# Optimization experiments

Measured on AMD Instinct MI355X. Metric: run time of the kernel, lower is better.

The kernel has to match this reference:

```python
import jax, jax.numpy as jnp
import numpy as np

B, N, DX, DZ = 4, 2048, 2, 128
PPD = (128, 128)
GRID_RANGE = ((-2.0, 2.0), (-2.0, 2.0))
INIT_LS = 0.1


def _construct_grid():
    axes = [jnp.linspace(lo, hi, p, dtype=jnp.float32) for (lo, hi), p in zip(GRID_RANGE, PPD)]
    mesh = jnp.meshgrid(*axes, indexing="ij")
    return jnp.stack(mesh, axis=-1)  # [128, 128, 2]


def setup_inputs() -> dict:
    key = jax.random.key(0)
    k1, k2 = jax.random.split(key)
    x = jax.random.uniform(k1, (B, N, DX), dtype=jnp.float32, minval=-2.0, maxval=2.0)
    z = jax.random.normal(k2, (B, N, DZ), dtype=jnp.float32)
    grid = _construct_grid()
    # inverse-softplus of init lengthscale, per dim
    ls0 = jnp.full((DX,), INIT_LS, dtype=jnp.float32)
    lengthscale_param = jnp.log(jnp.exp(ls0) - 1.0)
    return {"x": x, "z": z, "grid": grid, "lengthscale_param": lengthscale_param}


def reference(x, z, grid, lengthscale_param):
    b = x.shape[0]
    grid_shape = grid.shape[:-1]  # (128, 128)
    lengthscale = 1e-05 + jax.nn.softplus(lengthscale_param)  # [dx]
    grid_flat = grid.reshape(-1, grid.shape[-1])  # [M, dx], M = 16384
    # per-dim squared distance / l^2, summed over dx  -> [b, M, n]
    diff = grid_flat[None, :, None, :] - x[:, None, :, :]  # [b, M, n, dx]
    pre_exp = jnp.sum((diff * diff) / (lengthscale ** 2), axis=-1)
    weights = jnp.exp(-0.5 * pre_exp)  # [b, M, n]
    z_grid_flat = jnp.einsum("bmn,bnd->bmd", weights, z)  # [b, M, dz]
    z_grid = z_grid_flat.reshape((b,) + grid_shape + (z.shape[-1],))
    x_grid = jnp.broadcast_to(grid[None], (b,) + grid.shape)
    return (x_grid, z_grid)
```

## Files before the change

kernel.cpp:

```cpp
#include <hip/hip_runtime.h>

#define BATCH 4
#define NPTS  2048
#define DZDIM 128
#define GD    128
#define M_TOT (GD*GD)
#define TN    32
#define PZ    40
#define ZP    2112
#define WBIN  15

typedef __attribute__((ext_vector_type(8))) __bf16 bf16x8;
typedef __attribute__((ext_vector_type(4))) float floatx4;

__device__ __forceinline__ unsigned int f2bf_bits(float x){
  unsigned int u = __float_as_uint(x);
  u += 0x7FFFu + ((u >> 16) & 1u);
  return u >> 16;
}
__device__ __forceinline__ int point_bin(float px){
  int bin = __float2int_rn((px + 2.0f) * (127.0f / 4.0f));
  return min(GD - 1, max(0, bin));
}

__global__ __launch_bounds__(256) void prep_kernel(
    const float* __restrict__ x, const float* __restrict__ grid,
    float* __restrict__ out, int* __restrict__ binStart,
    float2* __restrict__ xs, int* __restrict__ perm)
{
  const int tid = threadIdx.x;
  if (blockIdx.x < BATCH){
    __shared__ int h[GD];
    __shared__ int s[GD + 1];
    const int b = blockIdx.x;
    const float2* __restrict__ x2 = (const float2*)x;
    if (tid < GD) h[tid] = 0;
    __syncthreads();
    float2 xv[8]; int bn[8];
#pragma unroll
    for (int u = 0; u < 8; ++u){
      xv[u] = x2[b*NPTS + u*256 + tid];
      bn[u] = point_bin(xv[u].x);
      atomicAdd(&h[bn[u]], 1);
    }
    __syncthreads();
    if (tid == 0){
      int acc = 0;
#pragma unroll
      for (int j = 0; j < GD; ++j){ s[j] = acc; acc += h[j]; }
      s[GD] = acc;
    }
    __syncthreads();
    if (tid <= GD) binStart[b*(GD+1) + tid] = s[tid];
    if (tid < GD) h[tid] = 0;
    __syncthreads();
#pragma unroll
    for (int u = 0; u < 8; ++u){
      int j = s[bn[u]] + atomicAdd(&h[bn[u]], 1);
      xs[(long)b*ZP + j]       = xv[u];
      perm[b*NPTS + j]         = u*256 + tid;
    }
  } else {
    int idx = (blockIdx.x - BATCH) * 256 + tid;
    float g = grid[idx];
#pragma unroll
    for (int bb = 0; bb < BATCH; ++bb) out[bb*(GD*GD*2) + idx] = g;
  }
}

__global__ __launch_bounds__(256) void ztwy_kernel(
    const float* __restrict__ z, const float2* __restrict__ xs,
    const int* __restrict__ perm, const float* __restrict__ lsp,
    unsigned short* __restrict__ zt, float* __restrict__ wy)
{
  const int b   = blockIdx.y;
  const int jj  = threadIdx.x & 31;
  const int oct = threadIdx.x >> 5;
  if (blockIdx.x >= NPTS/32){
    int j = NPTS + (blockIdx.x - NPTS/32)*32 + jj;
#pragma unroll
    for (int yy = 0; yy < 16; ++yy)
      wy[(long)(b*GD + oct*16 + yy)*ZP + j] = 0.f;
    return;
  }
  const int j = blockIdx.x*32 + jj;
  const int n = perm[b*NPTS + j];
  const float4* __restrict__ z4 = (const float4*)z;
  const long rb = (long)(b*NPTS + n) * 32;
#pragma unroll
  for (int r = 0; r < 4; ++r){
    int c = oct*4 + r;
    float4 v = z4[rb + c];
    long o = ((long)(b*DZDIM + 4*c) * ZP) + j;
    zt[o        ] = (unsigned short)f2bf_bits(v.x);
    zt[o +   ZP ] = (unsigned short)f2bf_bits(v.y);
    zt[o + 2*ZP ] = (unsigned short)f2bf_bits(v.z);
    zt[o + 3*ZP ] = (unsigned short)f2bf_bits(v.w);
  }
  const float l1 = 1e-5f + log1pf(expf(lsp[1]));
  const float c1 = -0.5f * 1.4426950408889634f / (l1*l1);
  const float step = 4.0f / 127.0f;
  const float y = xs[(long)b*ZP + j].y;
  float gy = -2.0f + (float)(oct*16) * step;
#pragma unroll
  for (int yy = 0; yy < 16; ++yy){
    float d = gy - y;
    wy[(long)(b*GD + oct*16 + yy)*ZP + j] = __builtin_amdgcn_exp2f(c1*d*d);
    gy += step;
  }
}

__global__ __launch_bounds__(256, 2) void setconv_mfma_kernel(
    const float2* __restrict__ xs, const int* __restrict__ binStart,
    const unsigned short* __restrict__ zt, const float* __restrict__ wy,
    const float* __restrict__ lsp, float* __restrict__ outz)
{
  __shared__ __align__(16) unsigned short Zlds[2][DZDIM * PZ];
  __shared__ __align__(16) float Wx[2][TN];

  const int tid = threadIdx.x, lane = tid & 63, wv = tid >> 6;
  const int bid = blockIdx.x;
  const int g   = bid & 7;
  const int s   = bid >> 3;
  const int b   = s & 3;
  const int il  = s >> 2;
  const int i   = g*16 + il;

  const float l0 = 1e-5f + log1pf(expf(lsp[0]));
  const float c0 = -0.5f * 1.4426950408889634f / (l0*l0);
  const float step = 4.0f / 127.0f;
  const float gx   = -2.0f + (float)i * step;

  const int lo  = binStart[b*(GD+1) + max(0, i - WBIN)];
  const int hi  = binStart[b*(GD+1) + min(GD-1, i + WBIN) + 1];
  const int lo8 = lo & ~7;
  const int len = hi - lo8;
  const int T   = (len + TN - 1) / TN;

  int goff[3];
#pragma unroll
  for (int u = 0; u < 3; ++u){
    int gi = wv + 4*u;
    if (gi < 10){
      int pos = gi*64 + lane;
      int d = pos / 5, c = pos % 5;
      if (c > 3) c = 3;
      goff[u] = (b*DZDIM + d) * ZP + c*8;
    } else goff[u] = 0;
  }

  const int q  = lane >> 4;
  const int ml = lane & 15;
  const float* __restrict__ wyp = wy + (long)(b*GD + wv*16 + ml) * ZP + q*8;

  floatx4 acc[2][8];
#pragma unroll
  for (int hh = 0; hh < 2; ++hh)
#pragma unroll
    for (int tz = 0; tz < 8; ++tz) acc[hh][tz] = (floatx4){0.f, 0.f, 0.f, 0.f};

  auto stageZ = [&](int buf, int t){
    const int k0 = lo8 + t*TN;
#pragma unroll
    for (int u = 0; u < 3; ++u){
      int gi = wv + 4*u;
      if (gi < 10){
        const unsigned short* gp = zt + goff[u] + k0;
        __builtin_amdgcn_global_load_lds(
            (__attribute__((address_space(1))) void*)gp,
            (__attribute__((address_space(3))) void*)&Zlds[buf][gi*512],
            16, 0, 0);
      }
    }
  };
  auto stageWx = [&](int buf, int t){
    if (tid < TN){
      int ka = t*TN + tid;
      float2 xv = xs[(long)b*ZP + lo8 + ka];
      float d = gx - xv.x;
      float w = __builtin_amdgcn_exp2f(c0*d*d);
      Wx[buf][tid] = (ka < len) ? w : 0.f;
    }
  };

  if (T > 0){
    stageZ(0, 0);
    stageWx(0, 0);
    floatx4 wA0 = *(const floatx4*)(wyp + lo8);
    floatx4 wB0 = *(const floatx4*)(wyp + lo8 + 4);
    floatx4 wA1 = *(const floatx4*)(wyp + 64*ZP + lo8);
    floatx4 wB1 = *(const floatx4*)(wyp + 64*ZP + lo8 + 4);
    __syncthreads();
    for (int t = 0; t < T; ++t){
      const int cur = t & 1, nxt = 1 - cur;
      if (t + 1 < T){ stageZ(nxt, t + 1); stageWx(nxt, t + 1); }
      const int tp = (t + 1 < T) ? t + 1 : t;
      floatx4 nA0 = *(const floatx4*)(wyp + lo8 + tp*TN);
      floatx4 nB0 = *(const floatx4*)(wyp + lo8 + tp*TN + 4);
      floatx4 nA1 = *(const floatx4*)(wyp + 64*ZP + lo8 + tp*TN);
      floatx4 nB1 = *(const floatx4*)(wyp + 64*ZP + lo8 + tp*TN + 4);
      floatx4 wx0 = *(const floatx4*)&Wx[cur][q*8];
      floatx4 wx1 = *(const floatx4*)&Wx[cur][q*8 + 4];
      union { unsigned int u[4]; bf16x8 v; } A0, A1;
      {
        float p0 = wA0[0]*wx0[0], p1 = wA0[1]*wx0[1], p2 = wA0[2]*wx0[2], p3 = wA0[3]*wx0[3];
        float p4 = wB0[0]*wx1[0], p5 = wB0[1]*wx1[1], p6 = wB0[2]*wx1[2], p7 = wB0[3]*wx1[3];
        asm("v_cvt_pk_bf16_f32 %0, %1, %2" : "=v"(A0.u[0]) : "v"(p0), "v"(p1));
        asm("v_cvt_pk_bf16_f32 %0, %1, %2" : "=v"(A0.u[1]) : "v"(p2), "v"(p3));
        asm("v_cvt_pk_bf16_f32 %0, %1, %2" : "=v"(A0.u[2]) : "v"(p4), "v"(p5));
        asm("v_cvt_pk_bf16_f32 %0, %1, %2" : "=v"(A0.u[3]) : "v"(p6), "v"(p7));
      }
      {
        float p0 = wA1[0]*wx0[0], p1 = wA1[1]*wx0[1], p2 = wA1[2]*wx0[2], p3 = wA1[3]*wx0[3];
        float p4 = wB1[0]*wx1[0], p5 = wB1[1]*wx1[1], p6 = wB1[2]*wx1[2], p7 = wB1[3]*wx1[3];
        asm("v_cvt_pk_bf16_f32 %0, %1, %2" : "=v"(A1.u[0]) : "v"(p0), "v"(p1));
        asm("v_cvt_pk_bf16_f32 %0, %1, %2" : "=v"(A1.u[1]) : "v"(p2), "v"(p3));
        asm("v_cvt_pk_bf16_f32 %0, %1, %2" : "=v"(A1.u[2]) : "v"(p4), "v"(p5));
        asm("v_cvt_pk_bf16_f32 %0, %1, %2" : "=v"(A1.u[3]) : "v"(p6), "v"(p7));
      }
      bf16x8 af0 = A0.v, af1 = A1.v;
#pragma unroll
      for (int tz = 0; tz < 8; ++tz){
        bf16x8 bf = *(const bf16x8*)&Zlds[cur][(tz*16 + ml)*PZ + q*8];
        acc[0][tz] = __builtin_amdgcn_mfma_f32_16x16x32_bf16(af0, bf, acc[0][tz], 0, 0, 0);
        acc[1][tz] = __builtin_amdgcn_mfma_f32_16x16x32_bf16(af1, bf, acc[1][tz], 0, 0, 0);
      }
      __syncthreads();
      wA0 = nA0; wB0 = nB0; wA1 = nA1; wB1 = nB1;
    }
  }

#pragma unroll
  for (int hh = 0; hh < 2; ++hh){
    const long obase = ((long)(b*M_TOT + i*GD + hh*64 + wv*16 + q*4) << 7) + ml;
#pragma unroll
    for (int tz = 0; tz < 8; ++tz)
#pragma unroll
      for (int r = 0; r < 4; ++r)
        outz[obase + ((long)r << 7) + tz*16] = acc[hh][tz][r];
  }
}

extern "C" void kernel_launch(void* const* d_in, const int* in_sizes, int n_in,
                              void* d_out, int out_size, void* d_ws, size_t ws_size,
                              hipStream_t stream)
{
  const float* x    = (const float*)d_in[0];
  const float* z    = (const float*)d_in[1];
  const float* grid = (const float*)d_in[2];
  const float* lsp  = (const float*)d_in[3];
  float* out = (float*)d_out;

  char* ws = (char*)d_ws;
  int*            binStart = (int*)ws;
  int*            perm     = (int*)(ws + 2064);
  float2*         xs       = (float2*)(ws + 34832);
  unsigned short* zt       = (unsigned short*)(ws + 102416);
  float*          wy       = (float*)(ws + 2265104);

  hipLaunchKernelGGL(prep_kernel, dim3(BATCH + GD), dim3(256), 0, stream,
                     x, grid, out, binStart, xs, perm);
  hipLaunchKernelGGL(ztwy_kernel, dim3(NPTS/32 + 2, BATCH), dim3(256), 0, stream,
                     z, xs, perm, lsp, zt, wy);
  hipLaunchKernelGGL(setconv_mfma_kernel, dim3(GD*BATCH), dim3(256), 0, stream,
                     xs, binStart, zt, wy, lsp, out + BATCH*GD*GD*2);
}
```

Before: 106.6 us.

## Compute Gaussian weights on the fly inside MFMA kernel instead of precomputed wy table

Removes the precomputed y-direction weight table (written by the z-transpose kernel and streamed from global memory each tile). The main MFMA kernel now stages the sorted point coordinates into LDS and evaluates the full 2D Gaussian weight with one exp2 per element directly in registers. This trades global memory traffic of about 4.3 MB of wy writes and reads for extra exp2 and FMA work per MFMA tile. It also removes the zero-padding blocks from the preceding kernel.

```diff
diff --git a/kernel.cpp b/kernel.cpp
--- a/kernel.cpp
+++ b/kernel.cpp
@@ -68,21 +68,13 @@
   }
 }
 
-__global__ __launch_bounds__(256) void ztwy_kernel(
-    const float* __restrict__ z, const float2* __restrict__ xs,
-    const int* __restrict__ perm, const float* __restrict__ lsp,
-    unsigned short* __restrict__ zt, float* __restrict__ wy)
+__global__ __launch_bounds__(256) void ztbuild_kernel(
+    const float* __restrict__ z, const int* __restrict__ perm,
+    unsigned short* __restrict__ zt)
 {
   const int b   = blockIdx.y;
   const int jj  = threadIdx.x & 31;
   const int oct = threadIdx.x >> 5;
-  if (blockIdx.x >= NPTS/32){
-    int j = NPTS + (blockIdx.x - NPTS/32)*32 + jj;
-#pragma unroll
-    for (int yy = 0; yy < 16; ++yy)
-      wy[(long)(b*GD + oct*16 + yy)*ZP + j] = 0.f;
-    return;
-  }
   const int j = blockIdx.x*32 + jj;
   const int n = perm[b*NPTS + j];
   const float4* __restrict__ z4 = (const float4*)z;
@@ -97,26 +89,15 @@
     zt[o + 2*ZP ] = (unsigned short)f2bf_bits(v.z);
     zt[o + 3*ZP ] = (unsigned short)f2bf_bits(v.w);
   }
-  const float l1 = 1e-5f + log1pf(expf(lsp[1]));
-  const float c1 = -0.5f * 1.4426950408889634f / (l1*l1);
-  const float step = 4.0f / 127.0f;
-  const float y = xs[(long)b*ZP + j].y;
-  float gy = -2.0f + (float)(oct*16) * step;
-#pragma unroll
-  for (int yy = 0; yy < 16; ++yy){
-    float d = gy - y;
-    wy[(long)(b*GD + oct*16 + yy)*ZP + j] = __builtin_amdgcn_exp2f(c1*d*d);
-    gy += step;
-  }
 }
 
 __global__ __launch_bounds__(256, 2) void setconv_mfma_kernel(
     const float2* __restrict__ xs, const int* __restrict__ binStart,
-    const unsigned short* __restrict__ zt, const float* __restrict__ wy,
-    const float* __restrict__ lsp, float* __restrict__ outz)
+    const unsigned short* __restrict__ zt, const float* __restrict__ lsp,
+    float* __restrict__ outz)
 {
   __shared__ __align__(16) unsigned short Zlds[2][DZDIM * PZ];
-  __shared__ __align__(16) float Wx[2][TN];
+  __shared__ __align__(16) float2 XS[2][TN];
 
   const int tid = threadIdx.x, lane = tid & 63, wv = tid >> 6;
   const int bid = blockIdx.x;
@@ -127,7 +108,10 @@
   const int i   = g*16 + il;
 
   const float l0 = 1e-5f + log1pf(expf(lsp[0]));
-  const float c0 = -0.5f * 1.4426950408889634f / (l0*l0);
+  const float l1 = 1e-5f + log1pf(expf(lsp[1]));
+  const float LOG2E = 1.4426950408889634f;
+  const float c0 = -0.5f * LOG2E / (l0*l0);
+  const float c1 = -0.5f * LOG2E / (l1*l1);
   const float step = 4.0f / 127.0f;
   const float gx   = -2.0f + (float)i * step;
 
@@ -151,7 +135,8 @@
 
   const int q  = lane >> 4;
   const int ml = lane & 15;
-  const float* __restrict__ wyp = wy + (long)(b*GD + wv*16 + ml) * ZP + q*8;
+  const float gy0 = -2.0f + (float)(wv*16 + ml) * step;
+  const float gy1 = gy0 + 64.0f * step;
 
   floatx4 acc[2][8];
 #pragma unroll
@@ -173,51 +158,40 @@
       }
     }
   };
-  auto stageWx = [&](int buf, int t){
-    if (tid < TN){
-      int ka = t*TN + tid;
-      float2 xv = xs[(long)b*ZP + lo8 + ka];
-      float d = gx - xv.x;
-      float w = __builtin_amdgcn_exp2f(c0*d*d);
-      Wx[buf][tid] = (ka < len) ? w : 0.f;
-    }
+  auto stageXS = [&](int buf, int t){
+    if (tid < TN)
+      XS[buf][tid] = xs[(long)b*ZP + lo8 + t*TN + tid];
   };
 
   if (T > 0){
     stageZ(0, 0);
-    stageWx(0, 0);
-    floatx4 wA0 = *(const floatx4*)(wyp + lo8);
-    floatx4 wB0 = *(const floatx4*)(wyp + lo8 + 4);
-    floatx4 wA1 = *(const floatx4*)(wyp + 64*ZP + lo8);
-    floatx4 wB1 = *(const floatx4*)(wyp + 64*ZP + lo8 + 4);
+    stageXS(0, 0);
     __syncthreads();
     for (int t = 0; t < T; ++t){
       const int cur = t & 1, nxt = 1 - cur;
-      if (t + 1 < T){ stageZ(nxt, t + 1); stageWx(nxt, t + 1); }
-      const int tp = (t + 1 < T) ? t + 1 : t;
-      floatx4 nA0 = *(const floatx4*)(wyp + lo8 + tp*TN);
-      floatx4 nB0 = *(const floatx4*)(wyp + lo8 + tp*TN + 4);
-      floatx4 nA1 = *(const floatx4*)(wyp + 64*ZP + lo8 + tp*TN);
-      floatx4 nB1 = *(const floatx4*)(wyp + 64*ZP + lo8 + tp*TN + 4);
-      floatx4 wx0 = *(const floatx4*)&Wx[cur][q*8];
-      floatx4 wx1 = *(const floatx4*)&Wx[cur][q*8 + 4];
+      if (t + 1 < T){ stageZ(nxt, t + 1); stageXS(nxt, t + 1); }
+      float w0[8], w1[8];
+#pragma unroll
+      for (int r = 0; r < 8; ++r){
+        float2 p = XS[cur][q*8 + r];
+        float dx = gx - p.x;
+        float t0 = c0*dx*dx;
+        float dy0 = gy0 - p.y, dy1 = gy1 - p.y;
+        float a0 = fmaf(c1*dy0, dy0, t0);
+        float a1 = fmaf(c1*dy1, dy1, t0);
+        bool ok = (t*TN + q*8 + r) < len;
+        w0[r] = ok ? __builtin_amdgcn_exp2f(a0) : 0.f;
+        w1[r] = ok ? __builtin_amdgcn_exp2f(a1) : 0.f;
+      }
       union { unsigned int u[4]; bf16x8 v; } A0, A1;
-      {
-        float p0 = wA0[0]*wx0[0], p1 = wA0[1]*wx0[1], p2 = wA0[2]*wx0[2], p3 = wA0[3]*wx0[3];
-        float p4 = wB0[0]*wx1[0], p5 = wB0[1]*wx1[1], p6 = wB0[2]*wx1[2], p7 = wB0[3]*wx1[3];
-        asm("v_cvt_pk_bf16_f32 %0, %1, %2" : "=v"(A0.u[0]) : "v"(p0), "v"(p1));
-        asm("v_cvt_pk_bf16_f32 %0, %1, %2" : "=v"(A0.u[1]) : "v"(p2), "v"(p3));
-        asm("v_cvt_pk_bf16_f32 %0, %1, %2" : "=v"(A0.u[2]) : "v"(p4), "v"(p5));
-        asm("v_cvt_pk_bf16_f32 %0, %1, %2" : "=v"(A0.u[3]) : "v"(p6), "v"(p7));
-      }
-      {
-        float p0 = wA1[0]*wx0[0], p1 = wA1[1]*wx0[1], p2 = wA1[2]*wx0[2], p3 = wA1[3]*wx0[3];
-        float p4 = wB1[0]*wx1[0], p5 = wB1[1]*wx1[1], p6 = wB1[2]*wx1[2], p7 = wB1[3]*wx1[3];
-        asm("v_cvt_pk_bf16_f32 %0, %1, %2" : "=v"(A1.u[0]) : "v"(p0), "v"(p1));
-        asm("v_cvt_pk_bf16_f32 %0, %1, %2" : "=v"(A1.u[1]) : "v"(p2), "v"(p3));
-        asm("v_cvt_pk_bf16_f32 %0, %1, %2" : "=v"(A1.u[2]) : "v"(p4), "v"(p5));
-        asm("v_cvt_pk_bf16_f32 %0, %1, %2" : "=v"(A1.u[3]) : "v"(p6), "v"(p7));
-      }
+      asm("v_cvt_pk_bf16_f32 %0, %1, %2" : "=v"(A0.u[0]) : "v"(w0[0]), "v"(w0[1]));
+      asm("v_cvt_pk_bf16_f32 %0, %1, %2" : "=v"(A0.u[1]) : "v"(w0[2]), "v"(w0[3]));
+      asm("v_cvt_pk_bf16_f32 %0, %1, %2" : "=v"(A0.u[2]) : "v"(w0[4]), "v"(w0[5]));
+      asm("v_cvt_pk_bf16_f32 %0, %1, %2" : "=v"(A0.u[3]) : "v"(w0[6]), "v"(w0[7]));
+      asm("v_cvt_pk_bf16_f32 %0, %1, %2" : "=v"(A1.u[0]) : "v"(w1[0]), "v"(w1[1]));
+      asm("v_cvt_pk_bf16_f32 %0, %1, %2" : "=v"(A1.u[1]) : "v"(w1[2]), "v"(w1[3]));
+      asm("v_cvt_pk_bf16_f32 %0, %1, %2" : "=v"(A1.u[2]) : "v"(w1[4]), "v"(w1[5]));
+      asm("v_cvt_pk_bf16_f32 %0, %1, %2" : "=v"(A1.u[3]) : "v"(w1[6]), "v"(w1[7]));
       bf16x8 af0 = A0.v, af1 = A1.v;
 #pragma unroll
       for (int tz = 0; tz < 8; ++tz){
@@ -226,7 +200,6 @@
         acc[1][tz] = __builtin_amdgcn_mfma_f32_16x16x32_bf16(af1, bf, acc[1][tz], 0, 0, 0);
       }
       __syncthreads();
-      wA0 = nA0; wB0 = nB0; wA1 = nA1; wB1 = nB1;
     }
   }
 
@@ -256,12 +229,11 @@
   int*            perm     = (int*)(ws + 2064);
   float2*         xs       = (float2*)(ws + 34832);
   unsigned short* zt       = (unsigned short*)(ws + 102416);
-  float*          wy       = (float*)(ws + 2265104);
 
   hipLaunchKernelGGL(prep_kernel, dim3(BATCH + GD), dim3(256), 0, stream,
                      x, grid, out, binStart, xs, perm);
-  hipLaunchKernelGGL(ztwy_kernel, dim3(NPTS/32 + 2, BATCH), dim3(256), 0, stream,
-                     z, xs, perm, lsp, zt, wy);
+  hipLaunchKernelGGL(ztbuild_kernel, dim3(NPTS/32, BATCH), dim3(256), 0, stream,
+                     z, perm, zt);
   hipLaunchKernelGGL(setconv_mfma_kernel, dim3(GD*BATCH), dim3(256), 0, stream,
-                     xs, binStart, zt, wy, lsp, out + BATCH*GD*GD*2);
-}
+                     xs, binStart, zt, lsp, out + BATCH*GD*GD*2);
+}
```

New measurement: 102.0 us. 4.3% less time.
